# Optimization experiments

Hardware: AMD Instinct MI355X
Metric: run time of the kernel (lower is better)

## Reference

```python
import jax, jax.numpy as jnp
import numpy as np

T_ITERS = 48  # number of unrolled PDHG iterations (init kwarg T)


def _grad3(u):
    """Forward-difference gradient with circular BC.
    u: (P, 1, X, Y, T) -> (P, 3, X, Y, T).
    conv with kernel (0,-1,1) + circular pad == roll(v,-1,axis) - v."""
    v = u[:, 0]
    return jnp.stack([jnp.roll(v, -1, axis=a) - v for a in (1, 2, 3)], axis=1)


def _grad3_adj(q):
    """Adjoint (negative divergence) with circular BC.
    q: (P, 3, X, Y, T) -> (P, 1, X, Y, T)."""
    out = sum(jnp.roll(q[:, d], 1, axis=d + 1) - q[:, d] for d in range(3))
    return out[:, None]


def setup_inputs() -> dict:
    key = jax.random.key(0)
    k1, k2 = jax.random.split(key)
    x = jax.random.normal(k1, (2, 1, 160, 160, 16), dtype=jnp.float32)
    # positive per-voxel regularization map, one per gradient direction
    lambda_map = jax.random.uniform(k2, (2, 3, 160, 160, 16), dtype=jnp.float32)
    return {"x": x, "lambda_map": lambda_map}


def reference(x, lambda_map):
    # op_norm_AHA = 1, op_norm_GHG = sqrt(12) -> L = sqrt(1 + 12)
    L = jnp.sqrt(jnp.asarray(13.0, x.dtype))
    s10 = jax.nn.sigmoid(jnp.asarray(10.0, x.dtype))  # sigmoid of init value 10.0
    sigma = s10 / L
    tau = s10 / L
    theta = s10

    xnoisy = x
    p = x
    q = jnp.zeros((x.shape[0], 3) + x.shape[2:], dtype=x.dtype)
    x0 = x
    xbar = x

    def step(carry, _):
        p, q, x0, xbar = carry
        p = (p + sigma * (xbar - xnoisy)) / (1.0 + sigma)
        q = jnp.clip(q + sigma * _grad3(xbar), -lambda_map, lambda_map)
        x1 = x0 - tau * p - tau * _grad3_adj(q)
        xbar = x1 + theta * (x1 - x0)
        return (p, q, x1, xbar), None

    (p, q, x1, xbar), _ = jax.lax.scan(step, (p, q, x0, xbar), None, length=T_ITERS)
    return x1
```

## Files before the change

### kernel.cpp

```cpp
#include <hip/hip_runtime.h>
#include <math.h>

#define XDIM 160
#define YDIM 160
#define TDIM 16
#define NB 2
#define T_ITERS 48
#define TILE 10
#define R1S 16
#define R0S 18
#define TPT (XDIM / TILE)
#define NTHR 512
#define NGRP (T_ITERS / 4)
#define FLAG_STRIDE 16

constexpr int VOL  = XDIM * YDIM * TDIM;
constexpr int NX   = NB * VOL;
constexpr int NBLK = NB * TPT * TPT;

typedef _Float16 hreal;
typedef _Float16 half4 __attribute__((ext_vector_type(4)));

__device__ __forceinline__ float clampl(float v, float l) {
    return fminf(fmaxf(v, -l), l);
}
__device__ __forceinline__ int wrap(int v) {
    return v < 0 ? v + XDIM : (v >= XDIM ? v - XDIM : v);
}
__device__ __forceinline__ int wrapT(int v) {
    return v < 0 ? v + TPT : (v >= TPT ? v - TPT : v);
}
__device__ __forceinline__ void ld4(const float* p, float* d) {
    float4 v = *(const float4*)p;
    d[0] = v.x; d[1] = v.y; d[2] = v.z; d[3] = v.w;
}
__device__ __forceinline__ void st4(float* p, const float* s) {
    *(float4*)p = make_float4(s[0], s[1], s[2], s[3]);
}
__device__ __forceinline__ void h2f4(const hreal* p, float* d) {
    half4 v = *(const half4*)p;
    d[0] = (float)v.x; d[1] = (float)v.y; d[2] = (float)v.z; d[3] = (float)v.w;
}
__device__ __forceinline__ float qrot_up(float x) {
    return __int_as_float(__builtin_amdgcn_update_dpp(
        0, __float_as_int(x), 0x39, 0xF, 0xF, true));
}
__device__ __forceinline__ float qrot_dn(float x) {
    return __int_as_float(__builtin_amdgcn_update_dpp(
        0, __float_as_int(x), 0x93, 0xF, 0xF, true));
}

__global__ __launch_bounds__(256) void init_kernel(
    const float* __restrict__ x, const float* __restrict__ lam,
    float* __restrict__ pA, float* __restrict__ xA,
    hreal* __restrict__ xbAh, hreal* __restrict__ qAh,
    hreal* __restrict__ lamh, hreal* __restrict__ xnh,
    unsigned* __restrict__ flags)
{
    int i = blockIdx.x * blockDim.x + threadIdx.x;
    if (i < NX) {
        float v = x[i];
        pA[i] = v; xA[i] = v;
        xbAh[i] = (hreal)v;
        xnh[i]  = (hreal)v;
    }
    if (i < 3 * NX) {
        qAh[i]  = (hreal)0.f;
        lamh[i] = (hreal)lam[i];
    }
    if (flags && i < NBLK * FLAG_STRIDE) flags[i] = 0u;
}

__global__ __launch_bounds__(NTHR, 4) void pd_persist(
    const hreal* __restrict__ xnh, const hreal* __restrict__ lamh,
    float* __restrict__ pA, float* __restrict__ pB,
    float* __restrict__ xA, float* __restrict__ xB,
    hreal* __restrict__ xbA, hreal* __restrict__ xbB,
    hreal* __restrict__ qA, hreal* __restrict__ qB,
    unsigned* __restrict__ flags,
    float sigma, float inv1ps, float tau, float theta)
{
    __shared__ float xbS[R0S * R0S * TDIM];
    __shared__ float q0S[(R1S + 1) * R1S * TDIM];
    __shared__ float q1S[R1S * (R1S + 1) * TDIM];

    const int tid = threadIdx.x;
    const int bid = blockIdx.x;
    const int b   = bid / (TPT * TPT);
    const int rem = bid % (TPT * TPT);
    const int tx  = rem / TPT, ty = rem % TPT;
    const int X0  = tx * TILE;
    const int Y0  = ty * TILE;
    const int xbase = b * VOL, qbase = b * 3 * VOL;
    const int t0 = (tid & 3) * 4;

    const unsigned* nbFlag = nullptr;
    if (tid < 8) {
        const int dxs[8] = {-1,-1,-1, 0, 0, 1, 1, 1};
        const int dys[8] = {-1, 0, 1,-1, 1,-1, 0, 1};
        int nx = wrapT(tx + dxs[tid]);
        int ny = wrapT(ty + dys[tid]);
        nbFlag = flags + (b * TPT * TPT + nx * TPT + ny) * FLAG_STRIDE;
    }

    float p[2][4], xv[2][4], xb[2][4], q0[2][4], q1[2][4], q2[2][4];
    half4 XNr[2], L0r[2], L1r[2], L2r[2];

    #pragma unroll
    for (int m = 0; m < 2; ++m) {
        int line = 128 * m + (tid >> 2);
        int lx = line >> 4, ly = line & 15;
        int gx = wrap(X0 - 3 + lx), gy = wrap(Y0 - 3 + ly);
        int off  = xbase + (gx * YDIM + gy) * TDIM + t0;
        int qoff = qbase + (gx * YDIM + gy) * TDIM + t0;
        XNr[m] = *(const half4*)(xnh + off);
        L0r[m] = *(const half4*)(lamh + qoff);
        L1r[m] = *(const half4*)(lamh + qoff + VOL);
        L2r[m] = *(const half4*)(lamh + qoff + 2 * VOL);
    }
    half4 LRr;
    if (tid < 64) {
        int rly = tid >> 2;
        LRr = *(const half4*)(lamh + qbase +
              (wrap(X0 - 4) * YDIM + wrap(Y0 - 3 + rly)) * TDIM + t0);
    } else if (tid < 128) {
        int rlx = (tid - 64) >> 2;
        LRr = *(const half4*)(lamh + qbase + VOL +
              (wrap(X0 - 3 + rlx) * YDIM + wrap(Y0 - 4)) * TDIM + t0);
    }

    #pragma unroll 1
    for (int g = 0; g < NGRP; ++g) {
        const bool e = (g & 1) == 0;
        const bool first = (g == 0);
        const bool fin   = (g == NGRP - 1);
        const float* __restrict__ pIn  = e ? pA : pB;
        float* __restrict__ pOut       = e ? pB : pA;
        const float* __restrict__ xIn  = e ? xA : xB;
        float* __restrict__ xOut       = e ? xB : xA;
        const hreal* __restrict__ xbIn = e ? xbA : xbB;
        hreal* __restrict__ xbOut      = e ? xbB : xbA;
        const hreal* __restrict__ qIn  = e ? qA : qB;
        hreal* __restrict__ qOut       = e ? qB : qA;

        if (!first) {
            if (tid < 8) {
                const unsigned tgt = (unsigned)g;
                for (unsigned it = 0; it < (1u << 22); ++it) {
                    if (__hip_atomic_load(nbFlag, __ATOMIC_ACQUIRE,
                                          __HIP_MEMORY_SCOPE_AGENT) >= tgt)
                        break;
                    __builtin_amdgcn_s_sleep(1);
                }
            }
            __syncthreads();
            __threadfence();
        }

        for (int s = tid; s < R0S * R0S * 4; s += NTHR) {
            int sq = s & 3, ln = s >> 2;
            int rx = ln / R0S, ry = ln % R0S;
            if (!first && rx >= 4 && rx < 14 && ry >= 4 && ry < 14) continue;
            int gx = wrap(X0 - 4 + rx), gy = wrap(Y0 - 4 + ry);
            float v[4];
            h2f4(xbIn + xbase + (gx * YDIM + gy) * TDIM + sq * 4, v);
            st4(xbS + ln * TDIM + sq * 4, v);
        }
        for (int s = tid; s < 17 * 16 * 4; s += NTHR) {
            int sq = s & 3, ln = s >> 2;
            int sx = ln / 16, sy = ln % 16;
            if (!first && sx >= 3 && sx < 14 && sy >= 3 && sy < 13) continue;
            int gx = wrap(X0 - 4 + sx), gy = wrap(Y0 - 3 + sy);
            float v[4];
            h2f4(qIn + qbase + (gx * YDIM + gy) * TDIM + sq * 4, v);
            st4(q0S + ln * TDIM + sq * 4, v);
        }
        for (int s = tid; s < 16 * 17 * 4; s += NTHR) {
            int sq = s & 3, ln = s >> 2;
            int sx = ln / 17, sy = ln % 17;
            if (!first && sx >= 3 && sx < 13 && sy >= 3 && sy < 14) continue;
            int gx = wrap(X0 - 3 + sx), gy = wrap(Y0 - 4 + sy);
            float v[4];
            h2f4(qIn + qbase + VOL + (gx * YDIM + gy) * TDIM + sq * 4, v);
            st4(q1S + ln * TDIM + sq * 4, v);
        }

        #pragma unroll
        for (int m = 0; m < 2; ++m) {
            int line = 128 * m + (tid >> 2);
            int lx = line >> 4, ly = line & 15;
            bool c = lx >= 3 && lx < 13 && ly >= 3 && ly < 13;
            if (first || !c) {
                int gx = wrap(X0 - 3 + lx), gy = wrap(Y0 - 3 + ly);
                int off  = xbase + (gx * YDIM + gy) * TDIM + t0;
                int qoff = qbase + (gx * YDIM + gy) * TDIM + t0;
                ld4(pIn + off, p[m]);
                ld4(xIn + off, xv[m]);
                h2f4(qIn + qoff + 2 * VOL, q2[m]);
            }
        }
        __syncthreads();
        #pragma unroll
        for (int m = 0; m < 2; ++m) {
            int line = 128 * m + (tid >> 2);
            int lx = line >> 4, ly = line & 15;
            bool c = lx >= 3 && lx < 13 && ly >= 3 && ly < 13;
            if (first || !c)
                ld4(xbS + ((lx + 1) * R0S + (ly + 1)) * TDIM + t0, xb[m]);
        }

        #pragma unroll
        for (int k = 1; k <= 4; ++k) {
            const int lo = k - 1, hi = 17 - k;

            if (k == 1) {
                if (tid < 64) {
                    int rly = tid >> 2;
                    float qr[4], xbc[4], xpx[4];
                    ld4(q0S + (0 * R1S + rly) * TDIM + t0, qr);
                    ld4(xbS + (0 * R0S + (rly + 1)) * TDIM + t0, xbc);
                    ld4(xbS + (1 * R0S + (rly + 1)) * TDIM + t0, xpx);
                    #pragma unroll
                    for (int j = 0; j < 4; ++j)
                        qr[j] = clampl(qr[j] + sigma * (xpx[j] - xbc[j]), (float)LRr[j]);
                    st4(q0S + (0 * R1S + rly) * TDIM + t0, qr);
                } else if (tid < 128) {
                    int rlx = (tid - 64) >> 2;
                    float qr[4], xbc[4], xpy[4];
                    ld4(q1S + (rlx * 17 + 0) * TDIM + t0, qr);
                    ld4(xbS + ((rlx + 1) * R0S + 0) * TDIM + t0, xbc);
                    ld4(xbS + ((rlx + 1) * R0S + 1) * TDIM + t0, xpy);
                    #pragma unroll
                    for (int j = 0; j < 4; ++j)
                        qr[j] = clampl(qr[j] + sigma * (xpy[j] - xbc[j]), (float)LRr[j]);
                    st4(q1S + (rlx * 17 + 0) * TDIM + t0, qr);
                }
            }

            #pragma unroll
            for (int m = 0; m < 2; ++m) {
                int line = 128 * m + (tid >> 2);
                int lx = line >> 4, ly = line & 15;
                bool inX = (lx >= lo && lx < hi), inY = (ly >= lo && ly < hi);
                bool aq0 = inY && (lx >= lo - 1) && (lx < hi);
                bool aq1 = inX && (ly >= lo - 1) && (ly < hi);
                bool ax  = inX && inY;

                if (k == 1) {
                    bool c = lx >= 3 && lx < 13 && ly >= 3 && ly < 13;
                    if (first || !c) {
                        ld4(q0S + ((lx + 1) * R1S + ly) * TDIM + t0, q0[m]);
                        ld4(q1S + (lx * 17 + (ly + 1)) * TDIM + t0, q1[m]);
                    }
                }
                if (aq0) {
                    float xpx[4];
                    ld4(xbS + ((lx + 2) * R0S + (ly + 1)) * TDIM + t0, xpx);
                    #pragma unroll
                    for (int j = 0; j < 4; ++j)
                        q0[m][j] = clampl(q0[m][j] + sigma * (xpx[j] - xb[m][j]),
                                          (float)L0r[m][j]);
                    st4(q0S + ((lx + 1) * R1S + ly) * TDIM + t0, q0[m]);
                }
                if (aq1) {
                    float xpy[4];
                    ld4(xbS + ((lx + 1) * R0S + (ly + 2)) * TDIM + t0, xpy);
                    #pragma unroll
                    for (int j = 0; j < 4; ++j)
                        q1[m][j] = clampl(q1[m][j] + sigma * (xpy[j] - xb[m][j]),
                                          (float)L1r[m][j]);
                    st4(q1S + (lx * 17 + (ly + 1)) * TDIM + t0, q1[m]);
                }
                if (ax) {
                    float xb_tp = qrot_up(xb[m][0]);
                    #pragma unroll
                    for (int j = 0; j < 4; ++j) {
                        float gt = ((j < 3) ? xb[m][j + 1] : xb_tp) - xb[m][j];
                        q2[m][j] = clampl(q2[m][j] + sigma * gt, (float)L2r[m][j]);
                        p[m][j]  = (p[m][j] + sigma * (xb[m][j] - (float)XNr[m][j]))
                                   * inv1ps;
                    }
                }
            }
            __syncthreads();

            #pragma unroll
            for (int m = 0; m < 2; ++m) {
                int line = 128 * m + (tid >> 2);
                int lx = line >> 4, ly = line & 15;
                bool ax = (lx >= lo && lx < hi && ly >= lo && ly < hi);
                if (ax) {
                    float q0b[4], q1b[4];
                    ld4(q0S + (lx * R1S + ly) * TDIM + t0, q0b);
                    ld4(q1S + (lx * 17 + ly) * TDIM + t0, q1b);
                    float q2tm = qrot_dn(q2[m][3]);
                    #pragma unroll
                    for (int j = 0; j < 4; ++j) {
                        float q2p = (j == 0) ? q2tm : q2[m][j - 1];
                        float div = (q0b[j] - q0[m][j]) + (q1b[j] - q1[m][j])
                                  + (q2p - q2[m][j]);
                        float xnew = xv[m][j] - tau * (p[m][j] + div);
                        xb[m][j] = xnew + theta * (xnew - xv[m][j]);
                        xv[m][j] = xnew;
                    }
                    st4(xbS + ((lx + 1) * R0S + (ly + 1)) * TDIM + t0, xb[m]);
                }
            }
            if (k < 4) __syncthreads();
        }

        #pragma unroll
        for (int m = 0; m < 2; ++m) {
            int line = 128 * m + (tid >> 2);
            int lx = line >> 4, ly = line & 15;
            if (lx >= 3 && lx < 13 && ly >= 3 && ly < 13) {
                int ox = lx - 3, oy = ly - 3;
                int gx = X0 + ox, gy = Y0 + oy;
                int off  = xbase + (gx * YDIM + gy) * TDIM + t0;
                int qoff = qbase + (gx * YDIM + gy) * TDIM + t0;
                if (fin) {
                    st4(xOut + off, xv[m]);
                } else {
                    bool px_skip = (ox >= 3 && ox < 7 && oy >= 3 && oy < 7);
                    bool q_skip  = (ox >= 4 && ox < 6 && oy >= 4 && oy < 6);
                    if (!px_skip) {
                        st4(pOut + off, p[m]);
                        st4(xOut + off, xv[m]);
                    }
                    if (!q_skip) {
                        half4 h;
                        h.x = (hreal)xb[m][0]; h.y = (hreal)xb[m][1];
                        h.z = (hreal)xb[m][2]; h.w = (hreal)xb[m][3];
                        *(half4*)(xbOut + off) = h;
                        h.x = (hreal)q0[m][0]; h.y = (hreal)q0[m][1];
                        h.z = (hreal)q0[m][2]; h.w = (hreal)q0[m][3];
                        *(half4*)(qOut + qoff) = h;
                        h.x = (hreal)q1[m][0]; h.y = (hreal)q1[m][1];
                        h.z = (hreal)q1[m][2]; h.w = (hreal)q1[m][3];
                        *(half4*)(qOut + qoff + VOL) = h;
                        h.x = (hreal)q2[m][0]; h.y = (hreal)q2[m][1];
                        h.z = (hreal)q2[m][2]; h.w = (hreal)q2[m][3];
                        *(half4*)(qOut + qoff + 2 * VOL) = h;
                    }
                }
            }
        }

        if (!fin) {
            __threadfence();
            __syncthreads();
            if (tid == 0)
                __hip_atomic_store(flags + bid * FLAG_STRIDE, (unsigned)(g + 1),
                                   __ATOMIC_RELEASE, __HIP_MEMORY_SCOPE_AGENT);
        }
    }
}

__global__ __launch_bounds__(NTHR, 4) void pd_step4(
    const hreal* __restrict__ xnh, const hreal* __restrict__ lamh,
    const float* __restrict__ pIn, float* __restrict__ pOut,
    const float* __restrict__ xIn, float* __restrict__ xOut,
    const hreal* __restrict__ xbIn, hreal* __restrict__ xbOut,
    const hreal* __restrict__ qIn, hreal* __restrict__ qOut,
    float sigma, float inv1ps, float tau, float theta)
{
    __shared__ float xbS[R0S * R0S * TDIM];
    __shared__ float q0S[(R1S + 1) * R1S * TDIM];
    __shared__ float q1S[R1S * (R1S + 1) * TDIM];

    const int tid = threadIdx.x;
    const int b   = blockIdx.x / (TPT * TPT);
    const int rem = blockIdx.x % (TPT * TPT);
    const int X0  = (rem / TPT) * TILE;
    const int Y0  = (rem % TPT) * TILE;
    const int xbase = b * VOL, qbase = b * 3 * VOL;

    const int qd = tid & 3, t0 = qd * 4;
    const int lane  = tid & 63;
    const int upSrc = (lane & 60) | ((lane + 1) & 3);
    const int dnSrc = (lane & 60) | ((lane + 3) & 3);

    for (int s = tid; s < R0S * R0S * 4; s += NTHR) {
        int sq = s & 3, ln = s >> 2;
        int rx = ln / R0S, ry = ln % R0S;
        int gx = wrap(X0 - 4 + rx), gy = wrap(Y0 - 4 + ry);
        float v[4];
        h2f4(xbIn + xbase + (gx * YDIM + gy) * TDIM + sq * 4, v);
        st4(xbS + ln * TDIM + sq * 4, v);
    }
    for (int s = tid; s < 17 * 16 * 4; s += NTHR) {
        int sq = s & 3, ln = s >> 2;
        int sx = ln / 16, sy = ln % 16;
        int gx = wrap(X0 - 4 + sx), gy = wrap(Y0 - 3 + sy);
        float v[4];
        h2f4(qIn + qbase + (gx * YDIM + gy) * TDIM + sq * 4, v);
        st4(q0S + ln * TDIM + sq * 4, v);
    }
    for (int s = tid; s < 16 * 17 * 4; s += NTHR) {
        int sq = s & 3, ln = s >> 2;
        int sx = ln / 17, sy = ln % 17;
        int gx = wrap(X0 - 3 + sx), gy = wrap(Y0 - 4 + sy);
        float v[4];
        h2f4(qIn + qbase + VOL + (gx * YDIM + gy) * TDIM + sq * 4, v);
        st4(q1S + ln * TDIM + sq * 4, v);
    }

    float p[2][4], xv[2][4], xb[2][4], q0[2][4], q1[2][4], q2[2][4];
    half4 XNr[2], L0r[2], L1r[2], L2r[2];
    #pragma unroll
    for (int m = 0; m < 2; ++m) {
        int line = 128 * m + (tid >> 2);
        int lx = line >> 4, ly = line & 15;
        int gx = wrap(X0 - 3 + lx), gy = wrap(Y0 - 3 + ly);
        int off  = xbase + (gx * YDIM + gy) * TDIM + t0;
        int qoff = qbase + (gx * YDIM + gy) * TDIM + t0;
        ld4(pIn + off, p[m]);
        ld4(xIn + off, xv[m]);
        h2f4(qIn + qoff + 2 * VOL, q2[m]);
        XNr[m] = *(const half4*)(xnh + off);
        L0r[m] = *(const half4*)(lamh + qoff);
        L1r[m] = *(const half4*)(lamh + qoff + VOL);
        L2r[m] = *(const half4*)(lamh + qoff + 2 * VOL);
    }

    half4 LRr;
    if (tid < 64) {
        int rly = tid >> 2;
        LRr = *(const half4*)(lamh + qbase +
              (wrap(X0 - 4) * YDIM + wrap(Y0 - 3 + rly)) * TDIM + t0);
    } else if (tid < 128) {
        int rlx = (tid - 64) >> 2;
        LRr = *(const half4*)(lamh + qbase + VOL +
              (wrap(X0 - 3 + rlx) * YDIM + wrap(Y0 - 4)) * TDIM + t0);
    }

    __syncthreads();

    #pragma unroll
    for (int m = 0; m < 2; ++m) {
        int line = 128 * m + (tid >> 2);
        int lx = line >> 4, ly = line & 15;
        ld4(xbS + ((lx + 1) * R0S + (ly + 1)) * TDIM + t0, xb[m]);
    }

    #pragma unroll
    for (int k = 1; k <= 4; ++k) {
        const int lo = k - 1, hi = 17 - k;

        if (k == 1) {
            if (tid < 64) {
                int rly = tid >> 2;
                float qr[4], xbc[4], xpx[4];
                ld4(q0S + (0 * R1S + rly) * TDIM + t0, qr);
                ld4(xbS + (0 * R0S + (rly + 1)) * TDIM + t0, xbc);
                ld4(xbS + (1 * R0S + (rly + 1)) * TDIM + t0, xpx);
                #pragma unroll
                for (int j = 0; j < 4; ++j)
                    qr[j] = clampl(qr[j] + sigma * (xpx[j] - xbc[j]), (float)LRr[j]);
                st4(q0S + (0 * R1S + rly) * TDIM + t0, qr);
            } else if (tid < 128) {
                int rlx = (tid - 64) >> 2;
                float qr[4], xbc[4], xpy[4];
                ld4(q1S + (rlx * 17 + 0) * TDIM + t0, qr);
                ld4(xbS + ((rlx + 1) * R0S + 0) * TDIM + t0, xbc);
                ld4(xbS + ((rlx + 1) * R0S + 1) * TDIM + t0, xpy);
                #pragma unroll
                for (int j = 0; j < 4; ++j)
                    qr[j] = clampl(qr[j] + sigma * (xpy[j] - xbc[j]), (float)LRr[j]);
                st4(q1S + (rlx * 17 + 0) * TDIM + t0, qr);
            }
        }

        #pragma unroll
        for (int m = 0; m < 2; ++m) {
            int line = 128 * m + (tid >> 2);
            int lx = line >> 4, ly = line & 15;
            bool inX = (lx >= lo && lx < hi), inY = (ly >= lo && ly < hi);
            bool aq0 = inY && (lx >= lo - 1) && (lx < hi);
            bool aq1 = inX && (ly >= lo - 1) && (ly < hi);
            bool ax  = inX && inY;

            if (k == 1) {
                ld4(q0S + ((lx + 1) * R1S + ly) * TDIM + t0, q0[m]);
                ld4(q1S + (lx * 17 + (ly + 1)) * TDIM + t0, q1[m]);
            }
            if (aq0) {
                float xpx[4];
                ld4(xbS + ((lx + 2) * R0S + (ly + 1)) * TDIM + t0, xpx);
                #pragma unroll
                for (int j = 0; j < 4; ++j)
                    q0[m][j] = clampl(q0[m][j] + sigma * (xpx[j] - xb[m][j]),
                                      (float)L0r[m][j]);
                st4(q0S + ((lx + 1) * R1S + ly) * TDIM + t0, q0[m]);
            }
            if (aq1) {
                float xpy[4];
                ld4(xbS + ((lx + 1) * R0S + (ly + 2)) * TDIM + t0, xpy);
                #pragma unroll
                for (int j = 0; j < 4; ++j)
                    q1[m][j] = clampl(q1[m][j] + sigma * (xpy[j] - xb[m][j]),
                                      (float)L1r[m][j]);
                st4(q1S + (lx * 17 + (ly + 1)) * TDIM + t0, q1[m]);
            }
            if (ax) {
                float xb_tp = __shfl(xb[m][0], upSrc, 64);
                #pragma unroll
                for (int j = 0; j < 4; ++j) {
                    float gt = ((j < 3) ? xb[m][j + 1] : xb_tp) - xb[m][j];
                    q2[m][j] = clampl(q2[m][j] + sigma * gt, (float)L2r[m][j]);
                    p[m][j]  = (p[m][j] + sigma * (xb[m][j] - (float)XNr[m][j]))
                               * inv1ps;
                }
            }
        }
        __syncthreads();

        #pragma unroll
        for (int m = 0; m < 2; ++m) {
            int line = 128 * m + (tid >> 2);
            int lx = line >> 4, ly = line & 15;
            bool ax = (lx >= lo && lx < hi && ly >= lo && ly < hi);
            if (ax) {
                float q0b[4], q1b[4];
                ld4(q0S + (lx * R1S + ly) * TDIM + t0, q0b);
                ld4(q1S + (lx * 17 + ly) * TDIM + t0, q1b);
                float q2tm = __shfl(q2[m][3], dnSrc, 64);
                #pragma unroll
                for (int j = 0; j < 4; ++j) {
                    float q2p = (j == 0) ? q2tm : q2[m][j - 1];
                    float div = (q0b[j] - q0[m][j]) + (q1b[j] - q1[m][j])
                              + (q2p - q2[m][j]);
                    float xnew = xv[m][j] - tau * (p[m][j] + div);
                    xb[m][j] = xnew + theta * (xnew - xv[m][j]);
                    xv[m][j] = xnew;
                }
                if (k < 4)
                    st4(xbS + ((lx + 1) * R0S + (ly + 1)) * TDIM + t0, xb[m]);
            }
        }
        if (k < 4) __syncthreads();
    }

    #pragma unroll
    for (int m = 0; m < 2; ++m) {
        int line = 128 * m + (tid >> 2);
        int lx = line >> 4, ly = line & 15;
        if (lx >= 3 && lx < 13 && ly >= 3 && ly < 13) {
            int gx = X0 + lx - 3, gy = Y0 + ly - 3;
            int off  = xbase + (gx * YDIM + gy) * TDIM + t0;
            int qoff = qbase + (gx * YDIM + gy) * TDIM + t0;
            st4(pOut + off, p[m]);
            st4(xOut + off, xv[m]);
            half4 h;
            h.x = (hreal)xb[m][0]; h.y = (hreal)xb[m][1];
            h.z = (hreal)xb[m][2]; h.w = (hreal)xb[m][3];
            *(half4*)(xbOut + off) = h;
            h.x = (hreal)q0[m][0]; h.y = (hreal)q0[m][1];
            h.z = (hreal)q0[m][2]; h.w = (hreal)q0[m][3];
            *(half4*)(qOut + qoff) = h;
            h.x = (hreal)q1[m][0]; h.y = (hreal)q1[m][1];
            h.z = (hreal)q1[m][2]; h.w = (hreal)q1[m][3];
            *(half4*)(qOut + qoff + VOL) = h;
            h.x = (hreal)q2[m][0]; h.y = (hreal)q2[m][1];
            h.z = (hreal)q2[m][2]; h.w = (hreal)q2[m][3];
            *(half4*)(qOut + qoff + 2 * VOL) = h;
        }
    }
}

extern "C" void kernel_launch(void* const* d_in, const int* in_sizes, int n_in,
                              void* d_out, int out_size, void* d_ws, size_t ws_size,
                              hipStream_t stream) {
    const float* x   = (const float*)d_in[0];
    const float* lam = (const float*)d_in[1];
    float* out = (float*)d_out;
    float* ws  = (float*)d_ws;

    float* pA  = ws;
    float* pB  = ws + (size_t)NX;
    float* xBb = ws + (size_t)2 * NX;
    float* xAb = out;
    hreal* hb  = (hreal*)(ws + (size_t)3 * NX);
    hreal* xbAh = hb;
    hreal* xbBh = hb + (size_t)NX;
    hreal* qAh  = hb + (size_t)2 * NX;
    hreal* qBh  = hb + (size_t)5 * NX;
    hreal* lamh = hb + (size_t)8 * NX;
    hreal* xnh  = hb + (size_t)11 * NX;
    unsigned* flags = (unsigned*)(ws + (size_t)9 * NX);

    const size_t ws_need = (size_t)9 * NX * sizeof(float)
                         + (size_t)NBLK * FLAG_STRIDE * sizeof(unsigned);

    const double s10 = 1.0 / (1.0 + exp(-10.0));
    const double L   = sqrt(13.0);
    float sigma  = (float)(s10 / L);
    float tau    = sigma;
    float theta  = (float)s10;
    float inv1ps = (float)(1.0 / (1.0 + s10 / L));

    static int persist_ok = -1;
    if (persist_ok < 0) {
        int nb = 0;
        hipError_t oe = hipOccupancyMaxActiveBlocksPerMultiprocessor(
            &nb, pd_persist, NTHR, 0);
        persist_ok = (oe == hipSuccess && nb >= 2) ? 1 : 0;
        (void)hipGetLastError();
    }
    const bool use_persist = persist_ok == 1 && ws_size >= ws_need;

    init_kernel<<<(3 * NX + 255) / 256, 256, 0, stream>>>(
        x, lam, pA, xAb, xbAh, qAh, lamh, xnh, use_persist ? flags : nullptr);

    if (use_persist) {
        pd_persist<<<NBLK, NTHR, 0, stream>>>(
            xnh, lamh, pA, pB, xAb, xBb, xbAh, xbBh, qAh, qBh, flags,
            sigma, inv1ps, tau, theta);
    } else {
        for (int j = 0; j < NGRP; ++j) {
            const bool e = (j & 1) == 0;
            pd_step4<<<NBLK, NTHR, 0, stream>>>(
                xnh, lamh,
                e ? pA : pB,   e ? pB : pA,
                e ? xAb : xBb, e ? xBb : xAb,
                e ? xbAh : xbBh, e ? xbBh : xbAh,
                e ? qAh : qBh,  e ? qBh : qAh,
                sigma, inv1ps, tau, theta);
        }
    }
}
```

Baseline: 252.4 us.

## Precompute halo ring load offsets, merge xbar/q buffers, remap block-to-tile order

The persistent kernel now precomputes per-thread global and LDS offsets for the halo ring exchange, replacing the three strided loops with a few unrolled predicated loads after the first group. The xbar and q half buffers are merged into one contiguous family per ping-pong side so that one base pointer is used. Shared memory becomes a single array, and per-line index math is hoisted out of the iteration loop. Block IDs are remapped so that neighbouring tiles fall into interleaved regions, which changes locality and scheduling of the flag waits. Register pressure rises from the cached offsets.

```diff
diff --git a/kernel.cpp b/kernel.cpp
--- a/kernel.cpp
+++ b/kernel.cpp
@@ -13,11 +13,16 @@
 #define NTHR 512
 #define NGRP (T_ITERS / 4)
 #define FLAG_STRIDE 16
+#define NRING 5
 
 constexpr int VOL  = XDIM * YDIM * TDIM;
 constexpr int NX   = NB * VOL;
 constexpr int NBLK = NB * TPT * TPT;
 
+constexpr int Q0B = R0S * R0S * TDIM;
+constexpr int Q1B = Q0B + 17 * 16 * TDIM;
+constexpr int SLDS = Q1B + 16 * 17 * TDIM;
+
 typedef _Float16 hreal;
 typedef _Float16 half4 __attribute__((ext_vector_type(4)));
 
@@ -53,7 +58,7 @@
 __global__ __launch_bounds__(256) void init_kernel(
     const float* __restrict__ x, const float* __restrict__ lam,
     float* __restrict__ pA, float* __restrict__ xA,
-    hreal* __restrict__ xbAh, hreal* __restrict__ qAh,
+    hreal* __restrict__ famA,
     hreal* __restrict__ lamh, hreal* __restrict__ xnh,
     unsigned* __restrict__ flags)
 {
@@ -61,11 +66,11 @@
     if (i < NX) {
         float v = x[i];
         pA[i] = v; xA[i] = v;
-        xbAh[i] = (hreal)v;
+        famA[i] = (hreal)v;
         xnh[i]  = (hreal)v;
     }
     if (i < 3 * NX) {
-        qAh[i]  = (hreal)0.f;
+        famA[NX + i] = (hreal)0.f;
         lamh[i] = (hreal)lam[i];
     }
     if (flags && i < NBLK * FLAG_STRIDE) flags[i] = 0u;
@@ -75,25 +80,23 @@
     const hreal* __restrict__ xnh, const hreal* __restrict__ lamh,
     float* __restrict__ pA, float* __restrict__ pB,
     float* __restrict__ xA, float* __restrict__ xB,
-    hreal* __restrict__ xbA, hreal* __restrict__ xbB,
-    hreal* __restrict__ qA, hreal* __restrict__ qB,
+    hreal* __restrict__ famA, hreal* __restrict__ famB,
     unsigned* __restrict__ flags,
     float sigma, float inv1ps, float tau, float theta)
 {
-    __shared__ float xbS[R0S * R0S * TDIM];
-    __shared__ float q0S[(R1S + 1) * R1S * TDIM];
-    __shared__ float q1S[R1S * (R1S + 1) * TDIM];
+    __shared__ float S[SLDS];
 
     const int tid = threadIdx.x;
-    const int bid = blockIdx.x;
-    const int b   = bid / (TPT * TPT);
-    const int rem = bid % (TPT * TPT);
-    const int tx  = rem / TPT, ty = rem % TPT;
-    const int X0  = tx * TILE;
-    const int Y0  = ty * TILE;
-    const int xbase = b * VOL, qbase = b * 3 * VOL;
+    const int region = blockIdx.x & 7;
+    const int local  = blockIdx.x >> 3;
+    const int b  = region >> 2;
+    const int tx = ((region >> 1) & 1) * 8 + (local >> 3);
+    const int ty = (region & 1) * 8 + (local & 7);
+    const int X0 = tx * TILE, Y0 = ty * TILE;
     const int t0 = (tid & 3) * 4;
-
+    const int QD = NX + 2 * b * VOL;
+
+    const int myFlag = b * TPT * TPT + tx * TPT + ty;
     const unsigned* nbFlag = nullptr;
     if (tid < 8) {
         const int dxs[8] = {-1,-1,-1, 0, 0, 1, 1, 1};
@@ -105,28 +108,78 @@
 
     float p[2][4], xv[2][4], xb[2][4], q0[2][4], q1[2][4], q2[2][4];
     half4 XNr[2], L0r[2], L1r[2], L2r[2];
+    int lx_[2], ly_[2], ro_[2], so_[2];
+    int a_xb[2], a_q0w[2], a_q1w[2];
+    bool c_[2], pxs_[2], qs_[2];
 
     #pragma unroll
     for (int m = 0; m < 2; ++m) {
         int line = 128 * m + (tid >> 2);
         int lx = line >> 4, ly = line & 15;
+        lx_[m] = lx; ly_[m] = ly;
         int gx = wrap(X0 - 3 + lx), gy = wrap(Y0 - 3 + ly);
-        int off  = xbase + (gx * YDIM + gy) * TDIM + t0;
-        int qoff = qbase + (gx * YDIM + gy) * TDIM + t0;
-        XNr[m] = *(const half4*)(xnh + off);
+        ro_[m] = b * VOL + (gx * YDIM + gy) * TDIM + t0;
+        so_[m] = b * VOL + ((X0 + lx - 3) * YDIM + (Y0 + ly - 3)) * TDIM + t0;
+        a_xb[m]  = ((lx + 1) * R0S + (ly + 1)) * TDIM + t0;
+        a_q0w[m] = Q0B + ((lx + 1) * 16 + ly) * TDIM + t0;
+        a_q1w[m] = Q1B + (lx * 17 + (ly + 1)) * TDIM + t0;
+        c_[m]   = lx >= 3 && lx < 13 && ly >= 3 && ly < 13;
+        int ox = lx - 3, oy = ly - 3;
+        pxs_[m] = (ox >= 3 && ox < 7 && oy >= 3 && oy < 7);
+        qs_[m]  = (ox >= 4 && ox < 6 && oy >= 4 && oy < 6);
+        int qoff = ro_[m] + 2 * b * VOL;
+        XNr[m] = *(const half4*)(xnh + ro_[m]);
         L0r[m] = *(const half4*)(lamh + qoff);
         L1r[m] = *(const half4*)(lamh + qoff + VOL);
         L2r[m] = *(const half4*)(lamh + qoff + 2 * VOL);
     }
     half4 LRr;
+    int rQ = 0, rXBC = 0;
     if (tid < 64) {
         int rly = tid >> 2;
-        LRr = *(const half4*)(lamh + qbase +
+        LRr = *(const half4*)(lamh + b * 3 * VOL +
               (wrap(X0 - 4) * YDIM + wrap(Y0 - 3 + rly)) * TDIM + t0);
+        rQ   = Q0B + rly * TDIM + t0;
+        rXBC = (rly + 1) * TDIM + t0;
     } else if (tid < 128) {
         int rlx = (tid - 64) >> 2;
-        LRr = *(const half4*)(lamh + qbase + VOL +
+        LRr = *(const half4*)(lamh + b * 3 * VOL + VOL +
               (wrap(X0 - 3 + rlx) * YDIM + wrap(Y0 - 4)) * TDIM + t0);
+        rQ   = Q1B + (rlx * 17) * TDIM + t0;
+        rXBC = ((rlx + 1) * R0S) * TDIM + t0;
+    }
+
+    int r_goff[NRING], r_loff[NRING];
+    #pragma unroll
+    for (int i = 0; i < NRING; ++i) {
+        int t = tid + NTHR * i;
+        int go = -1, lo = 0;
+        if (t < 896) {
+            int sq = t & 3, r = t >> 2, rx, ry;
+            if (r < 72)       { rx = r / 18; ry = r % 18; }
+            else if (r < 152) { int u = r - 72; rx = 4 + u / 8; int c = u % 8; ry = c < 4 ? c : c + 10; }
+            else              { int u = r - 152; rx = 14 + u / 18; ry = u % 18; }
+            int gx = wrap(X0 - 4 + rx), gy = wrap(Y0 - 4 + ry);
+            go = b * VOL + (gx * YDIM + gy) * TDIM + sq * 4;
+            lo = (rx * R0S + ry) * TDIM + sq * 4;
+        } else if (t < 1544) {
+            int v = t - 896; int sq = v & 3, r = v >> 2, sx, sy;
+            if (r < 48)       { sx = r / 16; sy = r % 16; }
+            else if (r < 114) { int u = r - 48; sx = 3 + u / 6; int c = u % 6; sy = c < 3 ? c : c + 10; }
+            else              { int u = r - 114; sx = 14 + u / 16; sy = u % 16; }
+            int gx = wrap(X0 - 4 + sx), gy = wrap(Y0 - 3 + sy);
+            go = NX + b * 3 * VOL + (gx * YDIM + gy) * TDIM + sq * 4;
+            lo = Q0B + (sx * 16 + sy) * TDIM + sq * 4;
+        } else if (t < 2192) {
+            int v = t - 1544; int sq = v & 3, r = v >> 2, sx, sy;
+            if (r < 51)       { sx = r / 17; sy = r % 17; }
+            else if (r < 111) { int u = r - 51; sx = 3 + u / 6; int c = u % 6; sy = c < 3 ? c : c + 11; }
+            else              { int u = r - 111; sx = 13 + u / 17; sy = u % 17; }
+            int gx = wrap(X0 - 3 + sx), gy = wrap(Y0 - 4 + sy);
+            go = NX + b * 3 * VOL + VOL + (gx * YDIM + gy) * TDIM + sq * 4;
+            lo = Q1B + (sx * 17 + sy) * TDIM + sq * 4;
+        }
+        r_goff[i] = go; r_loff[i] = lo;
     }
 
     #pragma unroll 1
@@ -138,10 +191,8 @@
         float* __restrict__ pOut       = e ? pB : pA;
         const float* __restrict__ xIn  = e ? xA : xB;
         float* __restrict__ xOut       = e ? xB : xA;
-        const hreal* __restrict__ xbIn = e ? xbA : xbB;
-        hreal* __restrict__ xbOut      = e ? xbB : xbA;
-        const hreal* __restrict__ qIn  = e ? qA : qB;
-        hreal* __restrict__ qOut       = e ? qB : qA;
+        const hreal* __restrict__ famIn = e ? famA : famB;
+        hreal* __restrict__ famOut      = e ? famB : famA;
 
         if (!first) {
             if (tid < 8) {
@@ -157,57 +208,55 @@
             __threadfence();
         }
 
-        for (int s = tid; s < R0S * R0S * 4; s += NTHR) {
-            int sq = s & 3, ln = s >> 2;
-            int rx = ln / R0S, ry = ln % R0S;
-            if (!first && rx >= 4 && rx < 14 && ry >= 4 && ry < 14) continue;
-            int gx = wrap(X0 - 4 + rx), gy = wrap(Y0 - 4 + ry);
-            float v[4];
-            h2f4(xbIn + xbase + (gx * YDIM + gy) * TDIM + sq * 4, v);
-            st4(xbS + ln * TDIM + sq * 4, v);
-        }
-        for (int s = tid; s < 17 * 16 * 4; s += NTHR) {
-            int sq = s & 3, ln = s >> 2;
-            int sx = ln / 16, sy = ln % 16;
-            if (!first && sx >= 3 && sx < 14 && sy >= 3 && sy < 13) continue;
-            int gx = wrap(X0 - 4 + sx), gy = wrap(Y0 - 3 + sy);
-            float v[4];
-            h2f4(qIn + qbase + (gx * YDIM + gy) * TDIM + sq * 4, v);
-            st4(q0S + ln * TDIM + sq * 4, v);
-        }
-        for (int s = tid; s < 16 * 17 * 4; s += NTHR) {
-            int sq = s & 3, ln = s >> 2;
-            int sx = ln / 17, sy = ln % 17;
-            if (!first && sx >= 3 && sx < 13 && sy >= 3 && sy < 14) continue;
-            int gx = wrap(X0 - 3 + sx), gy = wrap(Y0 - 4 + sy);
-            float v[4];
-            h2f4(qIn + qbase + VOL + (gx * YDIM + gy) * TDIM + sq * 4, v);
-            st4(q1S + ln * TDIM + sq * 4, v);
+        if (first) {
+            for (int s = tid; s < R0S * R0S * 4; s += NTHR) {
+                int sq = s & 3, ln = s >> 2;
+                int rx = ln / R0S, ry = ln % R0S;
+                int gx = wrap(X0 - 4 + rx), gy = wrap(Y0 - 4 + ry);
+                float v[4];
+                h2f4(famIn + b * VOL + (gx * YDIM + gy) * TDIM + sq * 4, v);
+                st4(S + ln * TDIM + sq * 4, v);
+            }
+            for (int s = tid; s < 17 * 16 * 4; s += NTHR) {
+                int sq = s & 3, ln = s >> 2;
+                int sx = ln / 16, sy = ln % 16;
+                int gx = wrap(X0 - 4 + sx), gy = wrap(Y0 - 3 + sy);
+                float v[4];
+                h2f4(famIn + NX + b * 3 * VOL + (gx * YDIM + gy) * TDIM + sq * 4, v);
+                st4(S + Q0B + ln * TDIM + sq * 4, v);
+            }
+            for (int s = tid; s < 16 * 17 * 4; s += NTHR) {
+                int sq = s & 3, ln = s >> 2;
+                int sx = ln / 17, sy = ln % 17;
+                int gx = wrap(X0 - 3 + sx), gy = wrap(Y0 - 4 + sy);
+                float v[4];
+                h2f4(famIn + NX + b * 3 * VOL + VOL + (gx * YDIM + gy) * TDIM + sq * 4, v);
+                st4(S + Q1B + ln * TDIM + sq * 4, v);
+            }
+        } else {
+            #pragma unroll
+            for (int i = 0; i < NRING; ++i) {
+                if (r_goff[i] >= 0) {
+                    float v[4];
+                    h2f4(famIn + r_goff[i], v);
+                    st4(S + r_loff[i], v);
+                }
+            }
         }
 
         #pragma unroll
         for (int m = 0; m < 2; ++m) {
-            int line = 128 * m + (tid >> 2);
-            int lx = line >> 4, ly = line & 15;
-            bool c = lx >= 3 && lx < 13 && ly >= 3 && ly < 13;
-            if (first || !c) {
-                int gx = wrap(X0 - 3 + lx), gy = wrap(Y0 - 3 + ly);
-                int off  = xbase + (gx * YDIM + gy) * TDIM + t0;
-                int qoff = qbase + (gx * YDIM + gy) * TDIM + t0;
-                ld4(pIn + off, p[m]);
-                ld4(xIn + off, xv[m]);
-                h2f4(qIn + qoff + 2 * VOL, q2[m]);
+            if (first || !c_[m]) {
+                ld4(pIn + ro_[m], p[m]);
+                ld4(xIn + ro_[m], xv[m]);
+                h2f4(famIn + ro_[m] + QD + 2 * VOL, q2[m]);
             }
         }
         __syncthreads();
         #pragma unroll
-        for (int m = 0; m < 2; ++m) {
-            int line = 128 * m + (tid >> 2);
-            int lx = line >> 4, ly = line & 15;
-            bool c = lx >= 3 && lx < 13 && ly >= 3 && ly < 13;
-            if (first || !c)
-                ld4(xbS + ((lx + 1) * R0S + (ly + 1)) * TDIM + t0, xb[m]);
-        }
+        for (int m = 0; m < 2; ++m)
+            if (first || !c_[m])
+                ld4(S + a_xb[m], xb[m]);
 
         #pragma unroll
         for (int k = 1; k <= 4; ++k) {
@@ -215,61 +264,55 @@
 
             if (k == 1) {
                 if (tid < 64) {
-                    int rly = tid >> 2;
                     float qr[4], xbc[4], xpx[4];
-                    ld4(q0S + (0 * R1S + rly) * TDIM + t0, qr);
-                    ld4(xbS + (0 * R0S + (rly + 1)) * TDIM + t0, xbc);
-                    ld4(xbS + (1 * R0S + (rly + 1)) * TDIM + t0, xpx);
+                    ld4(S + rQ, qr);
+                    ld4(S + rXBC, xbc);
+                    ld4(S + rXBC + R0S * TDIM, xpx);
                     #pragma unroll
                     for (int j = 0; j < 4; ++j)
                         qr[j] = clampl(qr[j] + sigma * (xpx[j] - xbc[j]), (float)LRr[j]);
-                    st4(q0S + (0 * R1S + rly) * TDIM + t0, qr);
+                    st4(S + rQ, qr);
                 } else if (tid < 128) {
-                    int rlx = (tid - 64) >> 2;
                     float qr[4], xbc[4], xpy[4];
-                    ld4(q1S + (rlx * 17 + 0) * TDIM + t0, qr);
-                    ld4(xbS + ((rlx + 1) * R0S + 0) * TDIM + t0, xbc);
-                    ld4(xbS + ((rlx + 1) * R0S + 1) * TDIM + t0, xpy);
+                    ld4(S + rQ, qr);
+                    ld4(S + rXBC, xbc);
+                    ld4(S + rXBC + TDIM, xpy);
                     #pragma unroll
                     for (int j = 0; j < 4; ++j)
                         qr[j] = clampl(qr[j] + sigma * (xpy[j] - xbc[j]), (float)LRr[j]);
-                    st4(q1S + (rlx * 17 + 0) * TDIM + t0, qr);
+                    st4(S + rQ, qr);
                 }
             }
 
             #pragma unroll
             for (int m = 0; m < 2; ++m) {
-                int line = 128 * m + (tid >> 2);
-                int lx = line >> 4, ly = line & 15;
+                int lx = lx_[m], ly = ly_[m];
                 bool inX = (lx >= lo && lx < hi), inY = (ly >= lo && ly < hi);
                 bool aq0 = inY && (lx >= lo - 1) && (lx < hi);
                 bool aq1 = inX && (ly >= lo - 1) && (ly < hi);
                 bool ax  = inX && inY;
 
-                if (k == 1) {
-                    bool c = lx >= 3 && lx < 13 && ly >= 3 && ly < 13;
-                    if (first || !c) {
-                        ld4(q0S + ((lx + 1) * R1S + ly) * TDIM + t0, q0[m]);
-                        ld4(q1S + (lx * 17 + (ly + 1)) * TDIM + t0, q1[m]);
-                    }
+                if (k == 1 && (first || !c_[m])) {
+                    ld4(S + a_q0w[m], q0[m]);
+                    ld4(S + a_q1w[m], q1[m]);
                 }
                 if (aq0) {
                     float xpx[4];
-                    ld4(xbS + ((lx + 2) * R0S + (ly + 1)) * TDIM + t0, xpx);
+                    ld4(S + a_xb[m] + R0S * TDIM, xpx);
                     #pragma unroll
                     for (int j = 0; j < 4; ++j)
                         q0[m][j] = clampl(q0[m][j] + sigma * (xpx[j] - xb[m][j]),
                                           (float)L0r[m][j]);
-                    st4(q0S + ((lx + 1) * R1S + ly) * TDIM + t0, q0[m]);
+                    st4(S + a_q0w[m], q0[m]);
                 }
                 if (aq1) {
                     float xpy[4];
-                    ld4(xbS + ((lx + 1) * R0S + (ly + 2)) * TDIM + t0, xpy);
+                    ld4(S + a_xb[m] + TDIM, xpy);
                     #pragma unroll
                     for (int j = 0; j < 4; ++j)
                         q1[m][j] = clampl(q1[m][j] + sigma * (xpy[j] - xb[m][j]),
                                           (float)L1r[m][j]);
-                    st4(q1S + (lx * 17 + (ly + 1)) * TDIM + t0, q1[m]);
+                    st4(S + a_q1w[m], q1[m]);
                 }
                 if (ax) {
                     float xb_tp = qrot_up(xb[m][0]);
@@ -286,13 +329,12 @@
 
             #pragma unroll
             for (int m = 0; m < 2; ++m) {
-                int line = 128 * m + (tid >> 2);
-                int lx = line >> 4, ly = line & 15;
+                int lx = lx_[m], ly = ly_[m];
                 bool ax = (lx >= lo && lx < hi && ly >= lo && ly < hi);
                 if (ax) {
                     float q0b[4], q1b[4];
-                    ld4(q0S + (lx * R1S + ly) * TDIM + t0, q0b);
-                    ld4(q1S + (lx * 17 + ly) * TDIM + t0, q1b);
+                    ld4(S + a_q0w[m] - 16 * TDIM, q0b);
+                    ld4(S + a_q1w[m] - TDIM, q1b);
                     float q2tm = qrot_dn(q2[m][3]);
                     #pragma unroll
                     for (int j = 0; j < 4; ++j) {
@@ -303,7 +345,7 @@
                         xb[m][j] = xnew + theta * (xnew - xv[m][j]);
                         xv[m][j] = xnew;
                     }
-                    st4(xbS + ((lx + 1) * R0S + (ly + 1)) * TDIM + t0, xb[m]);
+                    st4(S + a_xb[m], xb[m]);
                 }
             }
             if (k < 4) __syncthreads();
@@ -311,36 +353,29 @@
 
         #pragma unroll
         for (int m = 0; m < 2; ++m) {
-            int line = 128 * m + (tid >> 2);
-            int lx = line >> 4, ly = line & 15;
-            if (lx >= 3 && lx < 13 && ly >= 3 && ly < 13) {
-                int ox = lx - 3, oy = ly - 3;
-                int gx = X0 + ox, gy = Y0 + oy;
-                int off  = xbase + (gx * YDIM + gy) * TDIM + t0;
-                int qoff = qbase + (gx * YDIM + gy) * TDIM + t0;
+            if (c_[m]) {
+                int so = so_[m];
                 if (fin) {
-                    st4(xOut + off, xv[m]);
+                    st4(xOut + so, xv[m]);
                 } else {
-                    bool px_skip = (ox >= 3 && ox < 7 && oy >= 3 && oy < 7);
-                    bool q_skip  = (ox >= 4 && ox < 6 && oy >= 4 && oy < 6);
-                    if (!px_skip) {
-                        st4(pOut + off, p[m]);
-                        st4(xOut + off, xv[m]);
+                    if (!pxs_[m]) {
+                        st4(pOut + so, p[m]);
+                        st4(xOut + so, xv[m]);
                     }
-                    if (!q_skip) {
+                    if (!qs_[m]) {
                         half4 h;
                         h.x = (hreal)xb[m][0]; h.y = (hreal)xb[m][1];
                         h.z = (hreal)xb[m][2]; h.w = (hreal)xb[m][3];
-                        *(half4*)(xbOut + off) = h;
+                        *(half4*)(famOut + so) = h;
                         h.x = (hreal)q0[m][0]; h.y = (hreal)q0[m][1];
                         h.z = (hreal)q0[m][2]; h.w = (hreal)q0[m][3];
-                        *(half4*)(qOut + qoff) = h;
+                        *(half4*)(famOut + so + QD) = h;
                         h.x = (hreal)q1[m][0]; h.y = (hreal)q1[m][1];
                         h.z = (hreal)q1[m][2]; h.w = (hreal)q1[m][3];
-                        *(half4*)(qOut + qoff + VOL) = h;
+                        *(half4*)(famOut + so + QD + VOL) = h;
                         h.x = (hreal)q2[m][0]; h.y = (hreal)q2[m][1];
                         h.z = (hreal)q2[m][2]; h.w = (hreal)q2[m][3];
-                        *(half4*)(qOut + qoff + 2 * VOL) = h;
+                        *(half4*)(famOut + so + QD + 2 * VOL) = h;
                     }
                 }
             }
@@ -350,7 +385,7 @@
             __threadfence();
             __syncthreads();
             if (tid == 0)
-                __hip_atomic_store(flags + bid * FLAG_STRIDE, (unsigned)(g + 1),
+                __hip_atomic_store(flags + myFlag * FLAG_STRIDE, (unsigned)(g + 1),
                                    __ATOMIC_RELEASE, __HIP_MEMORY_SCOPE_AGENT);
         }
     }
@@ -365,8 +400,8 @@
     float sigma, float inv1ps, float tau, float theta)
 {
     __shared__ float xbS[R0S * R0S * TDIM];
-    __shared__ float q0S[(R1S + 1) * R1S * TDIM];
-    __shared__ float q1S[R1S * (R1S + 1) * TDIM];
+    __shared__ float q0S[17 * 16 * TDIM];
+    __shared__ float q1S[16 * 17 * TDIM];
 
     const int tid = threadIdx.x;
     const int b   = blockIdx.x / (TPT * TPT);
@@ -451,23 +486,23 @@
             if (tid < 64) {
                 int rly = tid >> 2;
                 float qr[4], xbc[4], xpx[4];
-                ld4(q0S + (0 * R1S + rly) * TDIM + t0, qr);
-                ld4(xbS + (0 * R0S + (rly + 1)) * TDIM + t0, xbc);
-                ld4(xbS + (1 * R0S + (rly + 1)) * TDIM + t0, xpx);
+                ld4(q0S + rly * TDIM + t0, qr);
+                ld4(xbS + (rly + 1) * TDIM + t0, xbc);
+                ld4(xbS + (R0S + rly + 1) * TDIM + t0, xpx);
                 #pragma unroll
                 for (int j = 0; j < 4; ++j)
                     qr[j] = clampl(qr[j] + sigma * (xpx[j] - xbc[j]), (float)LRr[j]);
-                st4(q0S + (0 * R1S + rly) * TDIM + t0, qr);
+                st4(q0S + rly * TDIM + t0, qr);
             } else if (tid < 128) {
                 int rlx = (tid - 64) >> 2;
                 float qr[4], xbc[4], xpy[4];
-                ld4(q1S + (rlx * 17 + 0) * TDIM + t0, qr);
-                ld4(xbS + ((rlx + 1) * R0S + 0) * TDIM + t0, xbc);
+                ld4(q1S + (rlx * 17) * TDIM + t0, qr);
+                ld4(xbS + ((rlx + 1) * R0S) * TDIM + t0, xbc);
                 ld4(xbS + ((rlx + 1) * R0S + 1) * TDIM + t0, xpy);
                 #pragma unroll
                 for (int j = 0; j < 4; ++j)
                     qr[j] = clampl(qr[j] + sigma * (xpy[j] - xbc[j]), (float)LRr[j]);
-                st4(q1S + (rlx * 17 + 0) * TDIM + t0, qr);
+                st4(q1S + (rlx * 17) * TDIM + t0, qr);
             }
         }
 
@@ -481,7 +516,7 @@
             bool ax  = inX && inY;
 
             if (k == 1) {
-                ld4(q0S + ((lx + 1) * R1S + ly) * TDIM + t0, q0[m]);
+                ld4(q0S + ((lx + 1) * 16 + ly) * TDIM + t0, q0[m]);
                 ld4(q1S + (lx * 17 + (ly + 1)) * TDIM + t0, q1[m]);
             }
             if (aq0) {
@@ -491,7 +526,7 @@
                 for (int j = 0; j < 4; ++j)
                     q0[m][j] = clampl(q0[m][j] + sigma * (xpx[j] - xb[m][j]),
                                       (float)L0r[m][j]);
-                st4(q0S + ((lx + 1) * R1S + ly) * TDIM + t0, q0[m]);
+                st4(q0S + ((lx + 1) * 16 + ly) * TDIM + t0, q0[m]);
             }
             if (aq1) {
                 float xpy[4];
@@ -522,7 +557,7 @@
             bool ax = (lx >= lo && lx < hi && ly >= lo && ly < hi);
             if (ax) {
                 float q0b[4], q1b[4];
-                ld4(q0S + (lx * R1S + ly) * TDIM + t0, q0b);
+                ld4(q0S + (lx * 16 + ly) * TDIM + t0, q0b);
                 ld4(q1S + (lx * 17 + ly) * TDIM + t0, q1b);
                 float q2tm = __shfl(q2[m][3], dnSrc, 64);
                 #pragma unroll
@@ -581,10 +616,8 @@
     float* xBb = ws + (size_t)2 * NX;
     float* xAb = out;
     hreal* hb  = (hreal*)(ws + (size_t)3 * NX);
-    hreal* xbAh = hb;
-    hreal* xbBh = hb + (size_t)NX;
-    hreal* qAh  = hb + (size_t)2 * NX;
-    hreal* qBh  = hb + (size_t)5 * NX;
+    hreal* famA = hb;
+    hreal* famB = hb + (size_t)4 * NX;
     hreal* lamh = hb + (size_t)8 * NX;
     hreal* xnh  = hb + (size_t)11 * NX;
     unsigned* flags = (unsigned*)(ws + (size_t)9 * NX);
@@ -610,11 +643,11 @@
     const bool use_persist = persist_ok == 1 && ws_size >= ws_need;
 
     init_kernel<<<(3 * NX + 255) / 256, 256, 0, stream>>>(
-        x, lam, pA, xAb, xbAh, qAh, lamh, xnh, use_persist ? flags : nullptr);
+        x, lam, pA, xAb, famA, lamh, xnh, use_persist ? flags : nullptr);
 
     if (use_persist) {
         pd_persist<<<NBLK, NTHR, 0, stream>>>(
-            xnh, lamh, pA, pB, xAb, xBb, xbAh, xbBh, qAh, qBh, flags,
+            xnh, lamh, pA, pB, xAb, xBb, famA, famB, flags,
             sigma, inv1ps, tau, theta);
     } else {
         for (int j = 0; j < NGRP; ++j) {
@@ -623,8 +656,8 @@
                 xnh, lamh,
                 e ? pA : pB,   e ? pB : pA,
                 e ? xAb : xBb, e ? xBb : xAb,
-                e ? xbAh : xbBh, e ? xbBh : xbAh,
-                e ? qAh : qBh,  e ? qBh : qAh,
+                e ? famA : famB, e ? famB : famA,
+                e ? famA + NX : famB + NX, e ? famB + NX : famA + NX,
                 sigma, inv1ps, tau, theta);
         }
     }
```

Measured after the change: 255.9 us. No clear change (+1.4%).
